# Performance work log

Hardware: AMD Instinct MI355X
Metric: run time of the kernel (lower is better)

The kernel has to match this reference:

```python
import jax, jax.numpy as jnp
import numpy as np


def setup_inputs() -> dict:
    key = jax.random.key(0)
    k1, k2 = jax.random.split(key)
    B, H, W, C = 16, 4, 900, 256
    input_1 = jax.random.normal(k1, (B, H, W, C), dtype=jnp.float32)
    input_2 = jax.random.normal(k2, (B, H, W, C), dtype=jnp.float32)
    return {"input_1": input_1, "input_2": input_2}


def reference(input_1, input_2):
    # Original op: circularly pad input_1 along W (shift by n_pad), frame into W
    # overlapping windows of length W, multiply by input_2 and sum over (H, W, C).
    # Equivalent math: out[b, s] = sum_w <x1[b, :, (s + w + n_pad) % W, :],
    #                                     x2[b, :, w, :]>  (inner product over H, C).
    # We compute the [B, W, W] Gram matrix with a GEMM, then reduce the circular
    # diagonal bands -- avoids materializing the W-times framed [B, H, W, W, C].
    B, H, W, C = input_1.shape
    n_pad = W // 2
    D = H * C
    a1 = jnp.transpose(input_1, (0, 2, 1, 3)).reshape(B, W, D)  # [B, W, H*C]
    a2 = jnp.transpose(input_2, (0, 2, 1, 3)).reshape(B, W, D)
    gram = jnp.einsum('bid,bjd->bij', a1, a2)  # gram[b, i, j] = <x1_i, x2_j>
    s = jnp.arange(W)[:, None]   # shift index
    w = jnp.arange(W)[None, :]   # window position
    idx = (s + w + n_pad) % W    # [W, W] circular gather indices
    out = jnp.sum(gram[:, idx, w], axis=-1)  # [B, W]
    return out
```

## Files before the change

### kernel.cpp

```cpp
#include <hip/hip_runtime.h>
#include <stdint.h>

typedef __attribute__((ext_vector_type(8))) short short8;
typedef __attribute__((ext_vector_type(4))) float floatx4;

#define W_DIM 900
#define PADW  1024
#define DDIM  1024
#define NPAD  450

__device__ __forceinline__ unsigned short f2bf(float f) {
  unsigned int u = __builtin_bit_cast(unsigned int, f);
  u += 0x7fffu + ((u >> 16) & 1u);
  return (unsigned short)(u >> 16);
}

__device__ __forceinline__ void async16(const void* g, void* l) {
  __builtin_amdgcn_global_load_lds(
      (const __attribute__((address_space(1))) void*)g,
      (__attribute__((address_space(3))) void*)l, 16, 0, 0);
}

__global__ void convert_kernel(const float* __restrict__ in1,
                               const float* __restrict__ in2,
                               unsigned short* __restrict__ dA,
                               unsigned short* __restrict__ dB) {
  const int w = blockIdx.x;
  const int b = blockIdx.y;
  const float* __restrict__ src = blockIdx.z ? in2 : in1;
  unsigned short* __restrict__ dst = blockIdx.z ? dB : dA;

  const int t  = threadIdx.x;
  const int h  = t >> 6;
  const int c4 = (t & 63) << 2;

  ushort4 o = make_ushort4(0, 0, 0, 0);
  if (w < W_DIM) {
    const size_t soff = (((size_t)(b * 4 + h) * W_DIM + w) * 256 + c4);
    float4 v = *reinterpret_cast<const float4*>(src + soff);
    o.x = f2bf(v.x); o.y = f2bf(v.y); o.z = f2bf(v.z); o.w = f2bf(v.w);
  }
  const size_t doff = ((size_t)b * PADW + w) * DDIM + h * 256 + c4;
  *reinterpret_cast<ushort4*>(dst + doff) = o;
}

__global__ void gemm_band_kernel(const unsigned short* __restrict__ A,
                                 const unsigned short* __restrict__ B,
                                 float* __restrict__ out) {
  const int b  = blockIdx.y;
  const int it = blockIdx.x >> 3;
  const int jt = blockIdx.x & 7;

  __shared__ __align__(16) unsigned char smem[64 * 132 * 4];
  unsigned short* As = (unsigned short*)smem;
  unsigned short* Bs = (unsigned short*)(smem + 8192);

  const int tid  = threadIdx.x;
  const int lane = tid & 63;
  const int warp = tid >> 6;
  const int wm   = warp >> 1;
  const int wn   = warp & 1;

  const unsigned short* Ab = A + ((size_t)(b * PADW + it * 128)) * DDIM;
  const unsigned short* Bb = B + ((size_t)(b * PADW + jt * 128)) * DDIM;

  const int srow = warp * 32 + (lane >> 2);
  const int scol = (lane & 3) * 8;
  const unsigned short* gA0 = Ab + (size_t)srow * DDIM + scol;
  const unsigned short* gA1 = gA0 + (size_t)16 * DDIM;
  const unsigned short* gB0 = Bb + (size_t)srow * DDIM + scol;
  const unsigned short* gB1 = gB0 + (size_t)16 * DDIM;
  unsigned short* lA0 = &As[srow * 32 + scol];
  unsigned short* lA1 = &As[(srow + 16) * 32 + scol];
  unsigned short* lB0 = &Bs[srow * 32 + scol];
  unsigned short* lB1 = &Bs[(srow + 16) * 32 + scol];

  floatx4 acc[4][4];
#pragma unroll
  for (int i = 0; i < 4; ++i)
#pragma unroll
    for (int j = 0; j < 4; ++j) acc[i][j] = (floatx4)0.0f;

  const int quad = lane >> 4;
  const int r16  = lane & 15;
  const unsigned short* ArowBase = &As[(wm * 64 + r16) * 32 + quad * 8];
  const unsigned short* BrowBase = &Bs[(wn * 64 + r16) * 32 + quad * 8];

  for (int kt = 0; kt < DDIM / 32; ++kt) {
    __syncthreads();
    const int ko = kt * 32;
    async16(gA0 + ko, lA0);
    async16(gA1 + ko, lA1);
    async16(gB0 + ko, lB0);
    async16(gB1 + ko, lB1);
    __syncthreads();

    short8 af[4], bf[4];
#pragma unroll
    for (int mi = 0; mi < 4; ++mi)
      af[mi] = *(const short8*)(ArowBase + mi * 16 * 32);
#pragma unroll
    for (int ni = 0; ni < 4; ++ni)
      bf[ni] = *(const short8*)(BrowBase + ni * 16 * 32);
#pragma unroll
    for (int mi = 0; mi < 4; ++mi)
#pragma unroll
      for (int ni = 0; ni < 4; ++ni)
        acc[mi][ni] = __builtin_amdgcn_mfma_f32_16x16x32_bf16(
            af[mi], bf[ni], acc[mi][ni], 0, 0, 0);
  }

  __syncthreads();
  float* Ep = (float*)smem;
  const int di_base = it * 128 - jt * 128 - NPAD;

  for (int half = 0; half < 2; ++half) {
    if (wm == half) {
#pragma unroll
      for (int mi = 0; mi < 4; ++mi)
#pragma unroll
        for (int ni = 0; ni < 4; ++ni)
#pragma unroll
          for (int r = 0; r < 4; ++r) {
            const int lr = mi * 16 + quad * 4 + r;
            const int c  = wn * 64 + ni * 16 + r16;
            Ep[lr * 132 + c] = acc[mi][ni][r];
          }
    }
    __syncthreads();
    if (tid < 191) {
      const int d = tid - 127;
      float s = 0.0f;
      for (int k = 0; k < 64; ++k) {
        const int j = k - d;
        if ((unsigned)j < 128u) s += Ep[k * 132 + j];
      }
      int dg = di_base + half * 64 + d;
      int sidx = dg % W_DIM;
      if (sidx < 0) sidx += W_DIM;
      atomicAdd(&out[b * W_DIM + sidx], s);
    }
    __syncthreads();
  }
}

__global__ void naive_kernel(const float* __restrict__ x1,
                             const float* __restrict__ x2,
                             float* __restrict__ out) {
  const int s = blockIdx.x;
  const int b = blockIdx.y;
  const int c = threadIdx.x;
  float acc = 0.0f;
  for (int h = 0; h < 4; ++h) {
    const float* p1 = x1 + (size_t)(b * 4 + h) * W_DIM * 256;
    const float* p2 = x2 + (size_t)(b * 4 + h) * W_DIM * 256;
    for (int w = 0; w < W_DIM; ++w) {
      int w1 = s + w + NPAD;
      if (w1 >= W_DIM) w1 -= W_DIM;
      if (w1 >= W_DIM) w1 -= W_DIM;
      acc += p1[(size_t)w1 * 256 + c] * p2[(size_t)w * 256 + c];
    }
  }
  for (int off = 32; off > 0; off >>= 1) acc += __shfl_down(acc, off, 64);
  __shared__ float red[4];
  if ((threadIdx.x & 63) == 0) red[threadIdx.x >> 6] = acc;
  __syncthreads();
  if (threadIdx.x == 0)
    out[b * W_DIM + s] = red[0] + red[1] + red[2] + red[3];
}

extern "C" void kernel_launch(void* const* d_in, const int* in_sizes, int n_in,
                              void* d_out, int out_size, void* d_ws, size_t ws_size,
                              hipStream_t stream) {
  const float* x1 = (const float*)d_in[0];
  const float* x2 = (const float*)d_in[1];
  float* out = (float*)d_out;

  hipMemsetAsync(d_out, 0, (size_t)out_size * sizeof(float), stream);

  const size_t need = (size_t)2 * 16 * PADW * DDIM * sizeof(unsigned short);
  if (ws_size >= need) {
    unsigned short* dA = (unsigned short*)d_ws;
    unsigned short* dB = dA + (size_t)16 * PADW * DDIM;
    convert_kernel<<<dim3(PADW, 16, 2), 256, 0, stream>>>(x1, x2, dA, dB);
    gemm_band_kernel<<<dim3(64, 16), 256, 0, stream>>>(dA, dB, out);
  } else {
    naive_kernel<<<dim3(W_DIM, 16), 256, 0, stream>>>(x1, x2, out);
  }
}
```

Measured before the change: 192.2 us.

## Enlarge GEMM tiles to 256x128 with BK 64 and widen conversion stores

The GEMM tile grows from 128x128 to 256x128 with a 64-wide K step, so each warp computes 8x4 MFMA fragments and global-to-LDS traffic per FLOP drops, with half as many barriers per unit of K. The band-reduction epilogue now runs in four passes and uses exact loop bounds instead of a per-element branch. The convert kernel handles two rows per block and writes 8 bf16 values per thread. In exchange there are fewer blocks (512 total) and higher register pressure from 128 accumulator floats, which can lower occupancy and leave CUs underused.

```diff
diff --git a/kernel.cpp b/kernel.cpp
--- a/kernel.cpp
+++ b/kernel.cpp
@@ -2,12 +2,16 @@
 #include <stdint.h>
 
 typedef __attribute__((ext_vector_type(8))) short short8;
+typedef __attribute__((ext_vector_type(8))) unsigned short ushort8;
 typedef __attribute__((ext_vector_type(4))) float floatx4;
 
 #define W_DIM 900
 #define PADW  1024
 #define DDIM  1024
 #define NPAD  450
+#define TM    256
+#define TN    128
+#define BK    64
 
 __device__ __forceinline__ unsigned short f2bf(float f) {
   unsigned int u = __builtin_bit_cast(unsigned int, f);
@@ -25,35 +29,39 @@
                                const float* __restrict__ in2,
                                unsigned short* __restrict__ dA,
                                unsigned short* __restrict__ dB) {
-  const int w = blockIdx.x;
-  const int b = blockIdx.y;
+  const int t  = threadIdx.x;
+  const int w  = blockIdx.x * 2 + (t >> 7);
+  const int b  = blockIdx.y;
   const float* __restrict__ src = blockIdx.z ? in2 : in1;
   unsigned short* __restrict__ dst = blockIdx.z ? dB : dA;
 
-  const int t  = threadIdx.x;
-  const int h  = t >> 6;
-  const int c4 = (t & 63) << 2;
-
-  ushort4 o = make_ushort4(0, 0, 0, 0);
+  const int tt = t & 127;
+  const int h  = tt >> 5;
+  const int c8 = (tt & 31) << 3;
+
+  ushort8 o = (ushort8)0;
   if (w < W_DIM) {
-    const size_t soff = (((size_t)(b * 4 + h) * W_DIM + w) * 256 + c4);
-    float4 v = *reinterpret_cast<const float4*>(src + soff);
-    o.x = f2bf(v.x); o.y = f2bf(v.y); o.z = f2bf(v.z); o.w = f2bf(v.w);
-  }
-  const size_t doff = ((size_t)b * PADW + w) * DDIM + h * 256 + c4;
-  *reinterpret_cast<ushort4*>(dst + doff) = o;
-}
-
-__global__ void gemm_band_kernel(const unsigned short* __restrict__ A,
-                                 const unsigned short* __restrict__ B,
-                                 float* __restrict__ out) {
+    const size_t soff = (((size_t)(b * 4 + h) * W_DIM + w) * 256 + c8);
+    float4 v0 = *reinterpret_cast<const float4*>(src + soff);
+    float4 v1 = *reinterpret_cast<const float4*>(src + soff + 4);
+    o[0] = f2bf(v0.x); o[1] = f2bf(v0.y); o[2] = f2bf(v0.z); o[3] = f2bf(v0.w);
+    o[4] = f2bf(v1.x); o[5] = f2bf(v1.y); o[6] = f2bf(v1.z); o[7] = f2bf(v1.w);
+  }
+  const size_t doff = ((size_t)b * PADW + w) * DDIM + h * 256 + c8;
+  *reinterpret_cast<ushort8*>(dst + doff) = o;
+}
+
+__global__ __launch_bounds__(256, 2)
+void gemm_band_kernel(const unsigned short* __restrict__ A,
+                      const unsigned short* __restrict__ B,
+                      float* __restrict__ out) {
   const int b  = blockIdx.y;
   const int it = blockIdx.x >> 3;
   const int jt = blockIdx.x & 7;
 
-  __shared__ __align__(16) unsigned char smem[64 * 132 * 4];
+  __shared__ __align__(16) unsigned char smem[49152];
   unsigned short* As = (unsigned short*)smem;
-  unsigned short* Bs = (unsigned short*)(smem + 8192);
+  unsigned short* Bs = (unsigned short*)smem + 16384;
 
   const int tid  = threadIdx.x;
   const int lane = tid & 63;
@@ -61,81 +69,94 @@
   const int wm   = warp >> 1;
   const int wn   = warp & 1;
 
-  const unsigned short* Ab = A + ((size_t)(b * PADW + it * 128)) * DDIM;
-  const unsigned short* Bb = B + ((size_t)(b * PADW + jt * 128)) * DDIM;
-
-  const int srow = warp * 32 + (lane >> 2);
-  const int scol = (lane & 3) * 8;
-  const unsigned short* gA0 = Ab + (size_t)srow * DDIM + scol;
-  const unsigned short* gA1 = gA0 + (size_t)16 * DDIM;
-  const unsigned short* gB0 = Bb + (size_t)srow * DDIM + scol;
-  const unsigned short* gB1 = gB0 + (size_t)16 * DDIM;
-  unsigned short* lA0 = &As[srow * 32 + scol];
-  unsigned short* lA1 = &As[(srow + 16) * 32 + scol];
-  unsigned short* lB0 = &Bs[srow * 32 + scol];
-  unsigned short* lB1 = &Bs[(srow + 16) * 32 + scol];
-
-  floatx4 acc[4][4];
-#pragma unroll
-  for (int i = 0; i < 4; ++i)
+  const unsigned short* Ab = A + ((size_t)(b * PADW + it * TM)) * DDIM;
+  const unsigned short* Bb = B + ((size_t)(b * PADW + jt * TN)) * DDIM;
+
+  const int r  = lane >> 2;
+  const int ch = (lane & 3) << 3;
+
+  const unsigned short* gA[8]; unsigned short* lA[8];
+#pragma unroll
+  for (int g = 0; g < 4; ++g)
+#pragma unroll
+    for (int s = 0; s < 2; ++s) {
+      const int row = warp * 64 + g * 16 + r;
+      gA[g * 2 + s] = Ab + (size_t)row * DDIM + s * 32 + ch;
+      lA[g * 2 + s] = As + s * 8192 + row * 32 + ch;
+    }
+  const unsigned short* gB[4]; unsigned short* lB[4];
+#pragma unroll
+  for (int g = 0; g < 2; ++g)
+#pragma unroll
+    for (int s = 0; s < 2; ++s) {
+      const int row = warp * 32 + g * 16 + r;
+      gB[g * 2 + s] = Bb + (size_t)row * DDIM + s * 32 + ch;
+      lB[g * 2 + s] = Bs + s * 4096 + row * 32 + ch;
+    }
+
+  floatx4 acc[8][4];
+#pragma unroll
+  for (int i = 0; i < 8; ++i)
 #pragma unroll
     for (int j = 0; j < 4; ++j) acc[i][j] = (floatx4)0.0f;
 
   const int quad = lane >> 4;
   const int r16  = lane & 15;
-  const unsigned short* ArowBase = &As[(wm * 64 + r16) * 32 + quad * 8];
-  const unsigned short* BrowBase = &Bs[(wn * 64 + r16) * 32 + quad * 8];
-
-  for (int kt = 0; kt < DDIM / 32; ++kt) {
-    __syncthreads();
-    const int ko = kt * 32;
-    async16(gA0 + ko, lA0);
-    async16(gA1 + ko, lA1);
-    async16(gB0 + ko, lB0);
-    async16(gB1 + ko, lB1);
-    __syncthreads();
-
-    short8 af[4], bf[4];
-#pragma unroll
-    for (int mi = 0; mi < 4; ++mi)
-      af[mi] = *(const short8*)(ArowBase + mi * 16 * 32);
-#pragma unroll
-    for (int ni = 0; ni < 4; ++ni)
-      bf[ni] = *(const short8*)(BrowBase + ni * 16 * 32);
-#pragma unroll
-    for (int mi = 0; mi < 4; ++mi)
+  const unsigned short* ArowBase = As + (wm * 128 + r16) * 32 + quad * 8;
+  const unsigned short* BrowBase = Bs + (wn * 64 + r16) * 32 + quad * 8;
+
+  for (int kt = 0; kt < DDIM / BK; ++kt) {
+    __syncthreads();
+    const int ko = kt * BK;
+#pragma unroll
+    for (int i = 0; i < 8; ++i) async16(gA[i] + ko, lA[i]);
+#pragma unroll
+    for (int i = 0; i < 4; ++i) async16(gB[i] + ko, lB[i]);
+    __syncthreads();
+
+    for (int kc = 0; kc < 2; ++kc) {
+      short8 af[8], bf[4];
+#pragma unroll
+      for (int mi = 0; mi < 8; ++mi)
+        af[mi] = *(const short8*)(ArowBase + kc * 8192 + mi * 16 * 32);
 #pragma unroll
       for (int ni = 0; ni < 4; ++ni)
-        acc[mi][ni] = __builtin_amdgcn_mfma_f32_16x16x32_bf16(
-            af[mi], bf[ni], acc[mi][ni], 0, 0, 0);
+        bf[ni] = *(const short8*)(BrowBase + kc * 4096 + ni * 16 * 32);
+#pragma unroll
+      for (int mi = 0; mi < 8; ++mi)
+#pragma unroll
+        for (int ni = 0; ni < 4; ++ni)
+          acc[mi][ni] = __builtin_amdgcn_mfma_f32_16x16x32_bf16(
+              af[mi], bf[ni], acc[mi][ni], 0, 0, 0);
+    }
   }
 
   __syncthreads();
   float* Ep = (float*)smem;
-  const int di_base = it * 128 - jt * 128 - NPAD;
-
-  for (int half = 0; half < 2; ++half) {
-    if (wm == half) {
-#pragma unroll
-      for (int mi = 0; mi < 4; ++mi)
+  const int dbase = it * TM - jt * TN - NPAD;
+
+  for (int p = 0; p < 4; ++p) {
+    if (wm == (p >> 1)) {
+      const int mib = (p & 1) * 4;
+#pragma unroll
+      for (int mo = 0; mo < 4; ++mo)
 #pragma unroll
         for (int ni = 0; ni < 4; ++ni)
 #pragma unroll
-          for (int r = 0; r < 4; ++r) {
-            const int lr = mi * 16 + quad * 4 + r;
+          for (int rr = 0; rr < 4; ++rr) {
+            const int lr = mo * 16 + quad * 4 + rr;
             const int c  = wn * 64 + ni * 16 + r16;
-            Ep[lr * 132 + c] = acc[mi][ni][r];
+            Ep[lr * 132 + c] = acc[mib + mo][ni][rr];
           }
     }
     __syncthreads();
     if (tid < 191) {
       const int d = tid - 127;
+      int k0 = d > 0 ? d : 0;
+      int k1 = 128 + d; if (k1 > 64) k1 = 64;
       float s = 0.0f;
-      for (int k = 0; k < 64; ++k) {
-        const int j = k - d;
-        if ((unsigned)j < 128u) s += Ep[k * 132 + j];
-      }
-      int dg = di_base + half * 64 + d;
+      for (int k = k0; k < k1; ++k) s += Ep[k * 132 + (k - d)];
+      int dg = dbase + p * 64 + d;
       int sidx = dg % W_DIM;
       if (sidx < 0) sidx += W_DIM;
       atomicAdd(&out[b * W_DIM + sidx], s);
@@ -182,8 +203,8 @@
   if (ws_size >= need) {
     unsigned short* dA = (unsigned short*)d_ws;
     unsigned short* dB = dA + (size_t)16 * PADW * DDIM;
-    convert_kernel<<<dim3(PADW, 16, 2), 256, 0, stream>>>(x1, x2, dA, dB);
-    gemm_band_kernel<<<dim3(64, 16), 256, 0, stream>>>(dA, dB, out);
+    convert_kernel<<<dim3(512, 16, 2), 256, 0, stream>>>(x1, x2, dA, dB);
+    gemm_band_kernel<<<dim3(32, 16), 256, 0, stream>>>(dA, dB, out);
   } else {
     naive_kernel<<<dim3(W_DIM, 16), 256, 0, stream>>>(x1, x2, out);
   }
```

Result: no change. 193.0 us (+0.4%).
